# Optimization experiments

Hardware: AMD Instinct MI355X
Metric: run time of the kernel (lower is better)

## Reference

```python
import jax, jax.numpy as jnp
import numpy as np

N_UP, N_DOWN, N_NUC, B = 16, 16, 8, 2048
EMB, TPS = 256, 32
N_ELEC = N_UP + N_DOWN


def mlp(x, w1, b1, w2, b2):
    # subnet: one hidden layer (tanh), linear output
    return jnp.tanh(x @ w1 + b1) @ w2 + b2


def _edge_indices():
    up = np.arange(N_UP)
    down = np.arange(N_UP, N_ELEC)

    def block_pairs(b):
        s, r = np.meshgrid(b, b, indexing='ij')
        m = s != r
        return s[m], r[m]

    s1, r1 = block_pairs(up)
    s2, r2 = block_pairs(down)
    senders_same = np.concatenate([s1, s2])
    receivers_same = np.concatenate([r1, r2])
    su, rd = np.meshgrid(up, down, indexing='ij')
    sd, ru = np.meshgrid(down, up, indexing='ij')
    senders_anti = np.concatenate([su.ravel(), sd.ravel()])
    receivers_anti = np.concatenate([rd.ravel(), ru.ravel()])
    senders_ne = np.repeat(np.arange(N_NUC), N_ELEC)
    receivers_ne = np.tile(np.arange(N_ELEC), N_NUC)
    return (senders_same, receivers_same, senders_anti, receivers_anti,
            senders_ne, receivers_ne)


def setup_inputs() -> dict:
    key = jax.random.key(0)
    ks = iter(jax.random.split(key, 32))

    def p(shape):
        return jax.random.normal(next(ks), shape, jnp.float32) * 0.1

    ss, rs, sa, ra, sn, rn = _edge_indices()
    inp = dict(
        electrons=p((B, N_ELEC, EMB)),
        nuclei=p((B, N_NUC, EMB)),
        feat_same=p((B, len(ss), TPS)),
        feat_anti=p((B, len(sa), TPS)),
        feat_ne=p((B, len(sn), TPS)),
        # u: per-edge-type deep-feature MLPs (TPS -> TPS)
        u_w1=p((3, TPS, TPS)), u_b1=jnp.zeros((3, TPS)),
        u_w2=p((3, TPS, TPS)), u_b2=jnp.zeros((3, TPS)),
        # w: per-edge-type message weight MLPs (TPS -> TPS)
        w_w1=p((3, TPS, TPS)), w_b1=jnp.zeros((3, TPS)),
        w_w2=p((3, TPS, TPS)), w_b2=jnp.zeros((3, TPS)),
        # h: per-edge-type sender-node MLPs (EMB -> TPS)
        h_w1=p((3, EMB, TPS)), h_b1=jnp.zeros((3, TPS)),
        h_w2=p((3, TPS, TPS)), h_b2=jnp.zeros((3, TPS)),
        # g: node update MLP (EMB + 3*TPS -> EMB), update_rule='concatenate'
        g_w1=p((EMB + 3 * TPS, EMB)), g_b1=jnp.zeros((EMB,)),
        g_w2=p((EMB, EMB)), g_b2=jnp.zeros((EMB,)),
        senders_same=jnp.asarray(ss, jnp.int32),
        receivers_same=jnp.asarray(rs, jnp.int32),
        senders_anti=jnp.asarray(sa, jnp.int32),
        receivers_anti=jnp.asarray(ra, jnp.int32),
        senders_ne=jnp.asarray(sn, jnp.int32),
        receivers_ne=jnp.asarray(rn, jnp.int32),
    )
    return inp


def reference(electrons, nuclei, feat_same, feat_anti, feat_ne,
              u_w1, u_b1, u_w2, u_b2,
              w_w1, w_b1, w_w2, w_b2,
              h_w1, h_b1, h_w2, h_b2,
              g_w1, g_b1, g_w2, g_b2,
              senders_same, receivers_same,
              senders_anti, receivers_anti,
              senders_ne, receivers_ne):
    feats = [feat_same, feat_anti, feat_ne]
    senders = [senders_same, senders_anti, senders_ne]
    receivers = [receivers_same, receivers_anti, receivers_ne]
    sender_nodes = [electrons, electrons, nuclei]
    z = []
    for t in range(3):  # fixed small set of edge types: same, anti, ne
        # deep features with two-particle residual (residual add)
        e = feats[t] + mlp(feats[t], u_w1[t], u_b1[t], u_w2[t], u_b2[t])
        we = mlp(e, w_w1[t], w_b1[t], w_w2[t], w_b2[t])              # [B, E_t, TPS]
        hx_nodes = mlp(sender_nodes[t], h_w1[t], h_b1[t], h_w2[t], h_b2[t])
        hx = hx_nodes[:, senders[t]]                                  # gather senders
        msg = we * hx
        # segment-sum over receivers into electron nodes
        zt = jnp.zeros((electrons.shape[0], N_ELEC, msg.shape[-1]), msg.dtype)
        z.append(zt.at[:, receivers[t]].add(msg))
    z_same, z_anti, z_ne = z
    # mean aggregation denominators (self_interaction=False -> self_mod=1)
    den_same = jnp.clip(jnp.concatenate(
        [jnp.full((N_UP, 1), N_UP - 1.0), jnp.full((N_DOWN, 1), N_DOWN - 1.0)]), 1.0)
    den_anti = jnp.clip(jnp.concatenate(
        [jnp.full((N_UP, 1), float(N_DOWN)), jnp.full((N_DOWN, 1), float(N_UP))]), 1.0)
    f = jnp.concatenate(
        [electrons, z_ne / N_NUC, z_same / den_same, z_anti / den_anti], axis=-1)
    updated = mlp(f, g_w1, g_b1, g_w2, g_b2)
    # one-particle residual (add)
    return electrons + updated
```

## Files before the change

### kernel.cpp

```cpp
#include <hip/hip_runtime.h>
#include <math.h>

#define NE 32
#define NN 8
#define EMB 256
#define TPS 32
#define E_SAME 480
#define E_ANTI 512
#define E_NE 256

#define AU1_OFF 0
#define AU2_OFF 3072
#define AW1_OFF 6144
#define AW2_OFF 9216
#define H1T_OFF 12288
#define H2T_OFF 36864
#define BIAS_OFF 39936
#define G1_OFF 40512
#define G2_OFF 130624

typedef float f32x4 __attribute__((ext_vector_type(4)));
typedef short s16x4 __attribute__((ext_vector_type(4)));
typedef short s16x8 __attribute__((ext_vector_type(8)));

__device__ __forceinline__ short f2bf(float x) {
    unsigned u = __builtin_bit_cast(unsigned, x);
    u += 0x7fffu + ((u >> 16) & 1u);
    return (short)(u >> 16);
}
__device__ __forceinline__ float bf2f(short h) {
    unsigned u = ((unsigned)(unsigned short)h) << 16;
    return __builtin_bit_cast(float, u);
}
__device__ __forceinline__ float fast_tanh(float x) {
    float e = __builtin_amdgcn_exp2f(x * 2.8853900817779268f);
    return 1.f - 2.f * __builtin_amdgcn_rcpf(e + 1.f);
}
__device__ __forceinline__ s16x8 pack8(float4 a, float4 b) {
    s16x8 r = { f2bf(a.x), f2bf(a.y), f2bf(a.z), f2bf(a.w),
                f2bf(b.x), f2bf(b.y), f2bf(b.z), f2bf(b.w) };
    return r;
}
__device__ __forceinline__ f32x4 mfma32(s16x8 a, s16x8 b, f32x4 c) {
    return __builtin_amdgcn_mfma_f32_16x16x32_bf16(a, b, c, 0, 0, 0);
}
__device__ __forceinline__ f32x4 mfma16(s16x4 a, s16x4 b, f32x4 c) {
#if __has_builtin(__builtin_amdgcn_mfma_f32_16x16x16bf16_1k)
    return __builtin_amdgcn_mfma_f32_16x16x16bf16_1k(a, b, c, 0, 0, 0);
#else
    asm volatile("v_mfma_f32_16x16x16_bf16 %0, %1, %2, %0" : "+v"(c) : "v"(a), "v"(b));
    return c;
#endif
}

__global__ void prep_weights(const float* __restrict__ u_w1, const float* __restrict__ u_w2,
                             const float* __restrict__ w_w1, const float* __restrict__ w_w2,
                             const float* __restrict__ h_w1, const float* __restrict__ h_w2,
                             const float* __restrict__ u_b1, const float* __restrict__ u_b2,
                             const float* __restrict__ w_b1, const float* __restrict__ w_b2,
                             const float* __restrict__ h_b1, const float* __restrict__ h_b2,
                             const float* __restrict__ g_w1, const float* __restrict__ g_w2,
                             short* __restrict__ wsb)
{
    int tile = blockIdx.x, lane = threadIdx.x;
    int g = lane >> 4, q = lane & 15;
    if (tile < 6) {
        int t = tile >> 1, mt = tile & 1;
        const float* src = u_w1 + t * 1024;
        short* dst = wsb + AU1_OFF + tile * 512 + lane * 8;
        #pragma unroll
        for (int i = 0; i < 8; ++i) dst[i] = f2bf(src[(8 * g + i) * 32 + mt * 16 + q]);
    } else if (tile < 42) {
        int m = (tile - 6) / 12, idx = (tile - 6) % 12;
        int mt = (idx >> 1) & 1, ks = idx & 1, t = idx >> 2;
        const float* mp = (m == 0) ? u_w2 : (m == 1) ? w_w1 : w_w2;
        const float* src = mp + t * 1024;
        short* dst = wsb + AU2_OFF + m * 3072 + idx * 256 + lane * 4;
        #pragma unroll
        for (int i = 0; i < 4; ++i) dst[i] = f2bf(src[(ks * 16 + 4 * g + i) * 32 + mt * 16 + q]);
    } else if (tile < 90) {
        int idx = tile - 42;
        int t = idx >> 4, r = idx & 15, mt = r >> 3, ks = r & 7;
        const float* src = h_w1 + t * 8192;
        short* dst = wsb + H1T_OFF + idx * 512 + lane * 8;
        #pragma unroll
        for (int i = 0; i < 8; ++i) dst[i] = f2bf(src[(ks * 32 + 8 * g + i) * 32 + mt * 16 + q]);
    } else if (tile < 102) {
        int idx = tile - 90;
        int t = idx >> 2, mt = (idx >> 1) & 1, ks = idx & 1;
        const float* src = h_w2 + t * 1024;
        short* dst = wsb + H2T_OFF + idx * 256 + lane * 4;
        #pragma unroll
        for (int i = 0; i < 4; ++i) dst[i] = f2bf(src[(ks * 16 + 4 * g + i) * 32 + mt * 16 + q]);
    } else if (tile == 102) {
        const float* bsrc[6] = {u_b1, u_b2, w_b1, w_b2, h_b1, h_b2};
        for (int j = lane; j < 576; j += 64)
            wsb[BIAS_OFF + j] = f2bf(bsrc[j / 96][j % 96]);
    } else if (tile < 279) {
        int idx = tile - 103, nt = idx / 11, ks = idx % 11;
        short* dst = wsb + G1_OFF + idx * 512 + lane * 8;
        #pragma unroll
        for (int i = 0; i < 8; ++i)
            dst[i] = f2bf(g_w1[(size_t)(ks * 32 + 8 * g + i) * 256 + nt * 16 + q]);
    } else {
        int idx = tile - 279;
        short* dst = wsb + G2_OFF + idx * 512 + lane * 8;
        int nt = idx >> 3, ks = idx & 7;
        #pragma unroll
        for (int i = 0; i < 8; ++i)
            dst[i] = f2bf(g_w2[(size_t)(ks * 32 + 8 * g + i) * 256 + nt * 16 + q]);
    }
}

#define LOAD_TILE(V0, V1, RL, RH, SE, RE, TIDX)                                   \
{                                                                                 \
    int ct_ = (TIDX) < real ? (TIDX) : real - 1;                                  \
    const float* fp_ = ft + ((size_t)b * cnt + ct_ * 16 + q) * TPS;               \
    V0 = *(const float4*)(fp_ + 8 * g);                                           \
    V1 = *(const float4*)(fp_ + 8 * g + 4);                                       \
    RL = *(const float4*)(fp_ + 4 * g);                                           \
    RH = *(const float4*)(fp_ + 16 + 4 * g);                                      \
    SE = snd[ct_ * 16 + q];                                                       \
    RE = rcv[ct_ * 16 + q];                                                       \
}

#define TILE_MLP(V0, V1, RL, RH, SE, RE, LIVE)                                    \
{                                                                                 \
    s16x8 B32 = pack8(V0, V1);                                                    \
    f32x4 c0 = {0.f,0.f,0.f,0.f}, c1 = {0.f,0.f,0.f,0.f};                         \
    c0 = mfma32(Au1_0, B32, c0);                                                  \
    c1 = mfma32(Au1_1, B32, c1);                                                  \
    s16x4 p0, p1;                                                                 \
    _Pragma("unroll")                                                             \
    for (int r = 0; r < 4; ++r) {                                                 \
        p0[r] = f2bf(fast_tanh(c0[r] + bf2f(bb1l[r])));                           \
        p1[r] = f2bf(fast_tanh(c1[r] + bf2f(bb1h[r])));                           \
    }                                                                             \
    f32x4 d0 = {0.f,0.f,0.f,0.f}, d1 = {0.f,0.f,0.f,0.f};                         \
    d0 = mfma16(Au2_[0], p0, d0); d0 = mfma16(Au2_[1], p1, d0);                   \
    d1 = mfma16(Au2_[2], p0, d1); d1 = mfma16(Au2_[3], p1, d1);                   \
    const float* rlp_ = (const float*)&RL; const float* rhp_ = (const float*)&RH; \
    _Pragma("unroll")                                                             \
    for (int r = 0; r < 4; ++r) {                                                 \
        p0[r] = f2bf(rlp_[r] + d0[r] + bf2f(bb2l[r]));                            \
        p1[r] = f2bf(rhp_[r] + d1[r] + bf2f(bb2h[r]));                            \
    }                                                                             \
    d0 = (f32x4){0.f,0.f,0.f,0.f}; d1 = (f32x4){0.f,0.f,0.f,0.f};                 \
    d0 = mfma16(Aw1_[0], p0, d0); d0 = mfma16(Aw1_[1], p1, d0);                   \
    d1 = mfma16(Aw1_[2], p0, d1); d1 = mfma16(Aw1_[3], p1, d1);                   \
    _Pragma("unroll")                                                             \
    for (int r = 0; r < 4; ++r) {                                                 \
        p0[r] = f2bf(fast_tanh(d0[r] + bf2f(bb3l[r])));                           \
        p1[r] = f2bf(fast_tanh(d1[r] + bf2f(bb3h[r])));                           \
    }                                                                             \
    d0 = (f32x4){0.f,0.f,0.f,0.f}; d1 = (f32x4){0.f,0.f,0.f,0.f};                 \
    d0 = mfma16(Aw2_[0], p0, d0); d0 = mfma16(Aw2_[1], p1, d0);                   \
    d1 = mfma16(Aw2_[2], p0, d1); d1 = mfma16(Aw2_[3], p1, d1);                   \
    if (LIVE) {                                                                   \
        s16x4 hlo = *(const s16x4*)(hxt + (SE) * 36 + 4 * g);                     \
        s16x4 hhi = *(const s16x4*)(hxt + (SE) * 36 + 16 + 4 * g);                \
        float* zr = z_s + (RE) * 97 + zc0 + 4 * g;                                \
        _Pragma("unroll")                                                         \
        for (int r = 0; r < 4; ++r) {                                             \
            atomicAdd(zr + r,      (d0[r] + bf2f(bb4l[r])) * bf2f(hlo[r]));       \
            atomicAdd(zr + 16 + r, (d1[r] + bf2f(bb4h[r])) * bf2f(hhi[r]));       \
        }                                                                         \
    }                                                                             \
}

__launch_bounds__(256, 2)
__global__ void gnn_kernel(
    const float* __restrict__ elec, const float* __restrict__ nuc,
    const float* __restrict__ fs,  const float* __restrict__ fa,  const float* __restrict__ fn,
    const float* __restrict__ g_b1, const float* __restrict__ g_b2,
    const int* __restrict__ ss, const int* __restrict__ rs,
    const int* __restrict__ sa, const int* __restrict__ ra,
    const int* __restrict__ sn, const int* __restrict__ rn,
    const short* __restrict__ wsb,
    float* __restrict__ out)
{
    __shared__ __align__(16) char smem[40384];
    short* f_s  = (short*)smem;
    float* z_s  = (float*)(smem + 22784);
    short* hx_s = (short*)(smem + 35200);
    short* H_s  = (short*)(smem + 22784);

    const int tid  = threadIdx.x;
    const int b    = blockIdx.x;
    const int lane = tid & 63, wv = tid >> 6;
    const int g    = lane >> 4, q = lane & 15;

    if (wv > 0)
        for (int i = tid - 64; i < 32 * 97; i += 192) z_s[i] = 0.f;

    #pragma unroll 1
    for (int task = wv; task < 5; task += 4) {
        int t, nt;
        if (task < 4) { t = task >> 1; nt = task & 1; }
        else          { t = 2; nt = 0; }
        const float* rowp = (t < 2) ? elec + ((size_t)b * NE + nt * 16 + q) * EMB
                                    : nuc  + ((size_t)b * NN + (q < 8 ? q : 7)) * EMB;
        f32x4 c0 = {0.f, 0.f, 0.f, 0.f}, c1 = {0.f, 0.f, 0.f, 0.f};
        const short* wA = wsb + H1T_OFF + t * 16 * 512;
        #pragma unroll
        for (int ks = 0; ks < 8; ++ks) {
            float4 v0 = *(const float4*)(rowp + 32 * ks + 8 * g);
            float4 v1 = *(const float4*)(rowp + 32 * ks + 8 * g + 4);
            s16x8 Bf = pack8(v0, v1);
            if (t == 0) {
                int off = (nt * 16 + q) * 356 + 32 * ks + 8 * g;
                *(s16x4*)(f_s + off)     = __builtin_shufflevector(Bf, Bf, 0, 1, 2, 3);
                *(s16x4*)(f_s + off + 4) = __builtin_shufflevector(Bf, Bf, 4, 5, 6, 7);
            }
            s16x8 a0 = *(const s16x8*)(wA + ks * 512 + lane * 8);
            s16x8 a1 = *(const s16x8*)(wA + (8 + ks) * 512 + lane * 8);
            c0 = mfma32(a0, Bf, c0);
            c1 = mfma32(a1, Bf, c1);
        }
        s16x4 b1l = *(const s16x4*)(wsb + BIAS_OFF + (12 + t) * 32 + 4 * g);
        s16x4 b1h = *(const s16x4*)(wsb + BIAS_OFF + (12 + t) * 32 + 16 + 4 * g);
        s16x4 p0, p1;
        #pragma unroll
        for (int r = 0; r < 4; ++r) {
            p0[r] = f2bf(fast_tanh(c0[r] + bf2f(b1l[r])));
            p1[r] = f2bf(fast_tanh(c1[r] + bf2f(b1h[r])));
        }
        const short* wA2 = wsb + H2T_OFF + t * 4 * 256;
        f32x4 d0 = {0.f, 0.f, 0.f, 0.f}, d1 = {0.f, 0.f, 0.f, 0.f};
        d0 = mfma16(*(const s16x4*)(wA2 + 0 * 256 + lane * 4), p0, d0);
        d0 = mfma16(*(const s16x4*)(wA2 + 1 * 256 + lane * 4), p1, d0);
        d1 = mfma16(*(const s16x4*)(wA2 + 2 * 256 + lane * 4), p0, d1);
        d1 = mfma16(*(const s16x4*)(wA2 + 3 * 256 + lane * 4), p1, d1);
        if (t < 2 || q < 8) {
            s16x4 b2l = *(const s16x4*)(wsb + BIAS_OFF + (15 + t) * 32 + 4 * g);
            s16x4 b2h = *(const s16x4*)(wsb + BIAS_OFF + (15 + t) * 32 + 16 + 4 * g);
            s16x4 w0, w1;
            #pragma unroll
            for (int r = 0; r < 4; ++r) {
                w0[r] = f2bf(d0[r] + bf2f(b2l[r]));
                w1[r] = f2bf(d1[r] + bf2f(b2h[r]));
            }
            int row = t * 32 + nt * 16 + q;
            *(s16x4*)(hx_s + row * 36 + 4 * g)      = w0;
            *(s16x4*)(hx_s + row * 36 + 16 + 4 * g) = w1;
        }
    }
    __syncthreads();

    #pragma unroll 1
    for (int t = 0; t < 3; ++t) {
        const float* ft; const int* snd; const int* rcv; int cnt, zc0;
        if (t == 0)      { ft = fs; snd = ss; rcv = rs; cnt = E_SAME; zc0 = 32; }
        else if (t == 1) { ft = fa; snd = sa; rcv = ra; cnt = E_ANTI; zc0 = 64; }
        else             { ft = fn; snd = sn; rcv = rn; cnt = E_NE;   zc0 = 0;  }
        s16x8 Au1_0 = *(const s16x8*)(wsb + AU1_OFF + (t * 2 + 0) * 512 + lane * 8);
        s16x8 Au1_1 = *(const s16x8*)(wsb + AU1_OFF + (t * 2 + 1) * 512 + lane * 8);
        s16x4 Au2_[4], Aw1_[4], Aw2_[4];
        #pragma unroll
        for (int i = 0; i < 4; ++i) {
            Au2_[i] = *(const s16x4*)(wsb + AU2_OFF + (t * 4 + i) * 256 + lane * 4);
            Aw1_[i] = *(const s16x4*)(wsb + AW1_OFF + (t * 4 + i) * 256 + lane * 4);
            Aw2_[i] = *(const s16x4*)(wsb + AW2_OFF + (t * 4 + i) * 256 + lane * 4);
        }
        s16x4 bb1l = *(const s16x4*)(wsb + BIAS_OFF + (0 + t) * 32 + 4 * g);
        s16x4 bb1h = *(const s16x4*)(wsb + BIAS_OFF + (0 + t) * 32 + 16 + 4 * g);
        s16x4 bb2l = *(const s16x4*)(wsb + BIAS_OFF + (3 + t) * 32 + 4 * g);
        s16x4 bb2h = *(const s16x4*)(wsb + BIAS_OFF + (3 + t) * 32 + 16 + 4 * g);
        s16x4 bb3l = *(const s16x4*)(wsb + BIAS_OFF + (6 + t) * 32 + 4 * g);
        s16x4 bb3h = *(const s16x4*)(wsb + BIAS_OFF + (6 + t) * 32 + 16 + 4 * g);
        s16x4 bb4l = *(const s16x4*)(wsb + BIAS_OFF + (9 + t) * 32 + 4 * g);
        s16x4 bb4h = *(const s16x4*)(wsb + BIAS_OFF + (9 + t) * 32 + 16 + 4 * g);
        const short* hxt = hx_s + t * 32 * 36;

        const int real  = cnt >> 4;
        const int npair = (real + 7) >> 3;

        #pragma unroll 1
        for (int j = 0; j < npair; ++j) {
            int tA = wv + 8 * j, tB = tA + 4;
            float4 v0A, v1A, rlA, rhA, v0B, v1B, rlB, rhB;
            int seA, reA, seB, reB;
            LOAD_TILE(v0A, v1A, rlA, rhA, seA, reA, tA);
            LOAD_TILE(v0B, v1B, rlB, rhB, seB, reB, tB);
            TILE_MLP(v0A, v1A, rlA, rhA, seA, reA, (tA < real));
            TILE_MLP(v0B, v1B, rlB, rhB, seB, reB, (tB < real));
        }
    }
    __syncthreads();

    for (int i = tid; i < 32 * 96; i += 256) {
        int r = i / 96, c = i - r * 96;
        float sc = (c < 32) ? 0.125f : ((c < 64) ? (1.f / 15.f) : (1.f / 16.f));
        f_s[r * 356 + 256 + c] = f2bf(z_s[r * 97 + c] * sc);
    }
    __syncthreads();

    #pragma unroll 1
    for (int task = wv; task < 32; task += 4) {
        int mt = task >> 4, nt = task & 15;
        f32x4 acc = {0.f, 0.f, 0.f, 0.f};
        const short* ar = f_s + (mt * 16 + q) * 356 + 8 * g;
        const short* wp = wsb + G1_OFF + nt * 11 * 512 + lane * 8;
        #pragma unroll
        for (int ks = 0; ks < 11; ++ks) {
            s16x4 alo = *(const s16x4*)(ar + 32 * ks);
            s16x4 ahi = *(const s16x4*)(ar + 32 * ks + 4);
            s16x8 a = __builtin_shufflevector(alo, ahi, 0, 1, 2, 3, 4, 5, 6, 7);
            s16x8 bw = *(const s16x8*)(wp + ks * 512);
            acc = mfma32(a, bw, acc);
        }
        float bias = g_b1[nt * 16 + q];
        #pragma unroll
        for (int r = 0; r < 4; ++r)
            H_s[(mt * 16 + 4 * g + r) * 260 + nt * 16 + q] = f2bf(fast_tanh(acc[r] + bias));
    }
    __syncthreads();

    #pragma unroll 1
    for (int task = wv; task < 32; task += 4) {
        int mt = task >> 4, nt = task & 15;
        f32x4 acc = {0.f, 0.f, 0.f, 0.f};
        const short* ar = H_s + (mt * 16 + q) * 260 + 8 * g;
        const short* wp = wsb + G2_OFF + nt * 8 * 512 + lane * 8;
        #pragma unroll
        for (int ks = 0; ks < 8; ++ks) {
            s16x4 alo = *(const s16x4*)(ar + 32 * ks);
            s16x4 ahi = *(const s16x4*)(ar + 32 * ks + 4);
            s16x8 a = __builtin_shufflevector(alo, ahi, 0, 1, 2, 3, 4, 5, 6, 7);
            s16x8 bw = *(const s16x8*)(wp + ks * 512);
            acc = mfma32(a, bw, acc);
        }
        float bias = g_b2[nt * 16 + q];
        #pragma unroll
        for (int r = 0; r < 4; ++r) {
            int row = mt * 16 + 4 * g + r, col = nt * 16 + q;
            size_t o = ((size_t)b * NE + row) * EMB + col;
            out[o] = bf2f(f_s[row * 356 + col]) + acc[r] + bias;
        }
    }
}

extern "C" void kernel_launch(void* const* d_in, const int* in_sizes, int n_in,
                              void* d_out, int out_size, void* d_ws, size_t ws_size,
                              hipStream_t stream) {
    const float* elec = (const float*)d_in[0];
    const float* nuc  = (const float*)d_in[1];
    const float* fs   = (const float*)d_in[2];
    const float* fa   = (const float*)d_in[3];
    const float* fn   = (const float*)d_in[4];
    const float* u_w1 = (const float*)d_in[5];
    const float* u_b1 = (const float*)d_in[6];
    const float* u_w2 = (const float*)d_in[7];
    const float* u_b2 = (const float*)d_in[8];
    const float* w_w1 = (const float*)d_in[9];
    const float* w_b1 = (const float*)d_in[10];
    const float* w_w2 = (const float*)d_in[11];
    const float* w_b2 = (const float*)d_in[12];
    const float* h_w1 = (const float*)d_in[13];
    const float* h_b1 = (const float*)d_in[14];
    const float* h_w2 = (const float*)d_in[15];
    const float* h_b2 = (const float*)d_in[16];
    const float* g_w1 = (const float*)d_in[17];
    const float* g_b1 = (const float*)d_in[18];
    const float* g_w2 = (const float*)d_in[19];
    const float* g_b2 = (const float*)d_in[20];
    const int* ss = (const int*)d_in[21];
    const int* rs = (const int*)d_in[22];
    const int* sa = (const int*)d_in[23];
    const int* ra = (const int*)d_in[24];
    const int* sn = (const int*)d_in[25];
    const int* rn = (const int*)d_in[26];

    short* wsb = (short*)d_ws;
    int nb = in_sizes[0] / (NE * EMB);

    prep_weights<<<407, 64, 0, stream>>>(u_w1, u_w2, w_w1, w_w2, h_w1, h_w2,
                                         u_b1, u_b2, w_b1, w_b2, h_b1, h_b2,
                                         g_w1, g_w2, wsb);
    gnn_kernel<<<nb, 256, 0, stream>>>(elec, nuc, fs, fa, fn, g_b1, g_b2,
                                       ss, rs, sa, ra, sn, rn, wsb, (float*)d_out);
}
```

Baseline: 489.9 us.

## Stage edge-feature tiles into LDS via async global_load_lds triple-buffer ring

Replaces direct per-lane global loads of edge-feature tiles with a per-wave triple-buffered LDS ring filled by global_load_lds, prefetching two tiles ahead. Uses an XOR swizzle on the staged layout and explicit vmcnt waits so the loads overlap the per-tile MLP work. The aim is to hide global memory latency in the edge loop. In exchange shared memory grows to about 64 KB per block, which may reduce occupancy, and the hand-written vmcnt counts must match the outstanding loads, including the snd/rcv index loads.

```diff
diff --git a/kernel.cpp b/kernel.cpp
--- a/kernel.cpp
+++ b/kernel.cpp
@@ -36,9 +36,9 @@
     float e = __builtin_amdgcn_exp2f(x * 2.8853900817779268f);
     return 1.f - 2.f * __builtin_amdgcn_rcpf(e + 1.f);
 }
-__device__ __forceinline__ s16x8 pack8(float4 a, float4 b) {
-    s16x8 r = { f2bf(a.x), f2bf(a.y), f2bf(a.z), f2bf(a.w),
-                f2bf(b.x), f2bf(b.y), f2bf(b.z), f2bf(b.w) };
+__device__ __forceinline__ s16x8 pack8(f32x4 a, f32x4 b) {
+    s16x8 r = { f2bf(a[0]), f2bf(a[1]), f2bf(a[2]), f2bf(a[3]),
+                f2bf(b[0]), f2bf(b[1]), f2bf(b[2]), f2bf(b[3]) };
     return r;
 }
 __device__ __forceinline__ f32x4 mfma32(s16x8 a, s16x8 b, f32x4 c) {
@@ -52,6 +52,19 @@
     return c;
 #endif
 }
+
+#if __has_builtin(__builtin_amdgcn_global_load_lds)
+#define HAVE_GLL 1
+__device__ __forceinline__ void stage16(const void* g, void* l) {
+    __builtin_amdgcn_global_load_lds((const __attribute__((address_space(1))) void*)g,
+                                     (__attribute__((address_space(3))) void*)l, 16, 0, 0);
+}
+#else
+#define HAVE_GLL 0
+__device__ __forceinline__ void stage16(const void* g, void* l) {
+    *(f32x4*)l = *(const f32x4*)g;
+}
+#endif
 
 __global__ void prep_weights(const float* __restrict__ u_w1, const float* __restrict__ u_w2,
                              const float* __restrict__ w_w1, const float* __restrict__ w_w2,
@@ -110,18 +123,6 @@
         for (int i = 0; i < 8; ++i)
             dst[i] = f2bf(g_w2[(size_t)(ks * 32 + 8 * g + i) * 256 + nt * 16 + q]);
     }
-}
-
-#define LOAD_TILE(V0, V1, RL, RH, SE, RE, TIDX)                                   \
-{                                                                                 \
-    int ct_ = (TIDX) < real ? (TIDX) : real - 1;                                  \
-    const float* fp_ = ft + ((size_t)b * cnt + ct_ * 16 + q) * TPS;               \
-    V0 = *(const float4*)(fp_ + 8 * g);                                           \
-    V1 = *(const float4*)(fp_ + 8 * g + 4);                                       \
-    RL = *(const float4*)(fp_ + 4 * g);                                           \
-    RH = *(const float4*)(fp_ + 16 + 4 * g);                                      \
-    SE = snd[ct_ * 16 + q];                                                       \
-    RE = rcv[ct_ * 16 + q];                                                       \
 }
 
 #define TILE_MLP(V0, V1, RL, RH, SE, RE, LIVE)                                    \
@@ -179,7 +180,7 @@
     const short* __restrict__ wsb,
     float* __restrict__ out)
 {
-    __shared__ __align__(16) char smem[40384];
+    __shared__ __align__(16) char smem[64960];
     short* f_s  = (short*)smem;
     float* z_s  = (float*)(smem + 22784);
     short* hx_s = (short*)(smem + 35200);
@@ -189,6 +190,14 @@
     const int b    = blockIdx.x;
     const int lane = tid & 63, wv = tid >> 6;
     const int g    = lane >> 4, q = lane & 15;
+
+    const int loff1 = (lane * 16) ^ (((lane >> 3) & 7) << 4);
+    const int kq    = (q & 7) << 4;
+    const int av0 = (q * 128 + g * 32) ^ kq;
+    const int av1 = (q * 128 + g * 32 + 16) ^ kq;
+    const int arl = (q * 128 + g * 16) ^ kq;
+    const int arh = (q * 128 + 64 + g * 16) ^ kq;
+    char* ringBase = smem + 40384 + wv * 6144;
 
     if (wv > 0)
         for (int i = tid - 64; i < 32 * 97; i += 192) z_s[i] = 0.f;
@@ -204,8 +213,8 @@
         const short* wA = wsb + H1T_OFF + t * 16 * 512;
         #pragma unroll
         for (int ks = 0; ks < 8; ++ks) {
-            float4 v0 = *(const float4*)(rowp + 32 * ks + 8 * g);
-            float4 v1 = *(const float4*)(rowp + 32 * ks + 8 * g + 4);
+            f32x4 v0 = *(const f32x4*)(rowp + 32 * ks + 8 * g);
+            f32x4 v1 = *(const f32x4*)(rowp + 32 * ks + 8 * g + 4);
             s16x8 Bf = pack8(v0, v1);
             if (t == 0) {
                 int off = (nt * 16 + q) * 356 + 32 * ks + 8 * g;
@@ -272,19 +281,43 @@
         s16x4 bb4h = *(const s16x4*)(wsb + BIAS_OFF + (9 + t) * 32 + 16 + 4 * g);
         const short* hxt = hx_s + t * 32 * 36;
 
-        const int real  = cnt >> 4;
-        const int npair = (real + 7) >> 3;
+        const int real = cnt >> 4;
+        const int NT   = (real + 3) >> 2;
+        const char* ftb = (const char*)(ft + (size_t)b * cnt * TPS);
+
+        #define STAGE_LVL(L)                                                      \
+        {                                                                         \
+            int tl_ = wv + 4 * (L); if (tl_ >= real) tl_ = real - 1;              \
+            const char* s_ = ftb + (size_t)tl_ * 2048;                            \
+            char* d_ = ringBase + ((L) % 3) * 2048;                               \
+            stage16(s_ + loff1, d_ + lane * 16);                                  \
+            stage16(s_ + 1024 + loff1, d_ + 1024 + lane * 16);                    \
+        }
+
+        STAGE_LVL(0);
+        STAGE_LVL(1);
 
         #pragma unroll 1
-        for (int j = 0; j < npair; ++j) {
-            int tA = wv + 8 * j, tB = tA + 4;
-            float4 v0A, v1A, rlA, rhA, v0B, v1B, rlB, rhB;
-            int seA, reA, seB, reB;
-            LOAD_TILE(v0A, v1A, rlA, rhA, seA, reA, tA);
-            LOAD_TILE(v0B, v1B, rlB, rhB, seB, reB, tB);
-            TILE_MLP(v0A, v1A, rlA, rhA, seA, reA, (tA < real));
-            TILE_MLP(v0B, v1B, rlB, rhB, seB, reB, (tB < real));
-        }
+        for (int jj = 0; jj < NT; ++jj) {
+            int tile = wv + 4 * jj;
+            int live = (tile < real);
+            int ct   = live ? tile : real - 1;
+            int se = snd[ct * 16 + q], re = rcv[ct * 16 + q];
+            if (jj + 2 < NT) STAGE_LVL(jj + 2);
+#if HAVE_GLL
+            if (jj + 2 < NT)      asm volatile("s_waitcnt vmcnt(6)" ::: "memory");
+            else if (jj + 1 < NT) asm volatile("s_waitcnt vmcnt(4)" ::: "memory");
+            else                  asm volatile("s_waitcnt vmcnt(2)" ::: "memory");
+            __builtin_amdgcn_sched_barrier(0);
+#endif
+            const char* sb = ringBase + (jj % 3) * 2048;
+            f32x4 v0 = *(const f32x4*)(sb + av0);
+            f32x4 v1 = *(const f32x4*)(sb + av1);
+            f32x4 rl = *(const f32x4*)(sb + arl);
+            f32x4 rh = *(const f32x4*)(sb + arh);
+            TILE_MLP(v0, v1, rl, rh, se, re, live);
+        }
+        #undef STAGE_LVL
     }
     __syncthreads();
 
```

After: 531.5 us. 8.5% more time.
